# Optimization experiments

Measured on AMD Instinct MI355X. Metric: run time of the kernel, lower is better.

## Reference

```python
import jax, jax.numpy as jnp
import numpy as np
from jax import lax

COMMITMENT_COST = 0.25

def setup_inputs() -> dict:
    key = jax.random.key(0)
    k1, k2, k3, k4 = jax.random.split(key, 4)
    B, C, H, W, K = 32, 128, 32, 32, 8192
    return {
        "x": jax.random.normal(k1, (B, C, H, W), dtype=jnp.float32),
        "W_lin": jax.random.normal(k2, (C, C), dtype=jnp.float32) * (1.0 / np.sqrt(C)),
        "b_lin": jax.random.normal(k3, (C,), dtype=jnp.float32) * 0.01,
        "emb": jax.random.normal(k4, (K, C), dtype=jnp.float32),
    }

def reference(x, W_lin, b_lin, emb):
    B, C, H, W = x.shape
    K = emb.shape[0]
    # BCHW -> BHWC, then linear projection
    inp = jnp.transpose(x, (0, 2, 3, 1))          # [B,H,W,C]
    inp = inp @ W_lin.T + b_lin                   # nn.Linear
    flat = inp.reshape(-1, C)                     # [N,C], N=B*H*W
    # squared L2 distances to codebook: ||z||^2 + ||e||^2 - 2 z.e
    d = (jnp.sum(flat**2, axis=1, keepdims=True)
         + jnp.sum(emb**2, axis=1)
         - 2.0 * flat @ emb.T)                    # [N,K]
    idx = jnp.argmin(d, axis=1)                   # [N]
    quantized = emb[idx].reshape(inp.shape)       # gather == onehot @ emb
    e_latent = jnp.mean((lax.stop_gradient(quantized) - inp) ** 2)
    q_latent = jnp.mean((quantized - lax.stop_gradient(inp)) ** 2)
    loss = q_latent + COMMITMENT_COST * e_latent
    # straight-through estimator
    quantized_st = inp + lax.stop_gradient(quantized - inp)
    # perplexity from code usage histogram (== mean of one-hot encodings)
    counts = jnp.zeros((K,), dtype=flat.dtype).at[idx].add(1.0)
    avg_probs = counts / flat.shape[0]
    perplexity = jnp.exp(-jnp.sum(avg_probs * jnp.log(avg_probs + 1e-10)))
    out = jnp.transpose(quantized_st, (0, 3, 1, 2))  # back to BCHW
    return (loss, out, perplexity, idx[:, None])
```

## Files before the change

kernel.cpp:

```cpp
#include <hip/hip_runtime.h>
#include <hip/hip_bf16.h>
#include <float.h>

#define NPIX   32768
#define CDIM   128
#define KCB    8192
#define EPS_STOP 0.30f
#define TAUF   0.012f
#define RCAP   8192
#define RCAPA  2048

typedef _Float16 f16x8 __attribute__((ext_vector_type(8)));
typedef float    f32x16 __attribute__((ext_vector_type(16)));

#define WS_EMBFH   0
#define WS_E2      2359296
#define WS_ZWS     2392064
#define WS_CAND    19169280
#define WS_IDX     20217856
#define WS_RLISTA  20348928
#define WS_RLISTB  20381696
#define WS_SCAND   20512768
#define WS_SCANI   21037056
#define WS_COUNTS  21299200
#define WS_LOSS    21331968
#define WS_RCNTA   21331972
#define WS_RCNTB   21331976
#define WS_ZERO_OFF 21299200
#define WS_ZERO_LEN 32780

#define OUT_OFF_OUT  1
#define OUT_OFF_PERP 4194305
#define OUT_OFF_IDX  4194306

__device__ __forceinline__ void ins6(float f, float v[6]) {
    float a = fmaxf(v[0], f); v[0] = fminf(v[0], f);
    float b = fmaxf(v[1], a); v[1] = fminf(v[1], a);
    a = fmaxf(v[2], b); v[2] = fminf(v[2], b);
    b = fmaxf(v[3], a); v[3] = fminf(v[3], a);
    a = fmaxf(v[4], b); v[4] = fminf(v[4], b);
    v[5] = fminf(v[5], a);
}

__global__ __launch_bounds__(256) void k_e2(const float* __restrict__ emb, float* __restrict__ e2) {
    int t = threadIdx.x;
    int wv = t >> 6, l = t & 63;
    int k = blockIdx.x * 4 + wv;
    const float2 v = *(const float2*)&emb[(size_t)k * 128 + l * 2];
    float s = v.x * v.x + v.y * v.y;
    #pragma unroll
    for (int o = 32; o; o >>= 1) s += __shfl_down(s, o, 64);
    if (l == 0) e2[k] = s;
}

__global__ __launch_bounds__(256) void k_prep(const float* __restrict__ emb, const float* __restrict__ e2,
                                              _Float16* __restrict__ embFh) {
    int tid = blockIdx.x * 256 + threadIdx.x;
    int m = tid / 18, r = tid % 18;
    int s = r >> 1, h = r & 1;
    f16x8 hv;
    #pragma unroll
    for (int j = 0; j < 8; ++j) hv[j] = (_Float16)0.0f;
    if (s < 8) {
        int c0 = s * 16 + h * 8;
        const float4 a = *(const float4*)&emb[(size_t)m * 128 + c0];
        const float4 b = *(const float4*)&emb[(size_t)m * 128 + c0 + 4];
        float vals[8] = {a.x, a.y, a.z, a.w, b.x, b.y, b.z, b.w};
        #pragma unroll
        for (int j = 0; j < 8; ++j) hv[j] = (_Float16)(-2.0f * vals[j]);
    } else if (h == 0) {
        float v = e2[m] + 512.0f;
        _Float16 eh = (_Float16)v;
        hv[0] = eh;
        hv[1] = (_Float16)(v - (float)eh);
    }
    size_t base = (((size_t)(m >> 5) * 9 + s) * 64 + (m & 31) + h * 32) * 8;
    *(f16x8*)&embFh[base] = hv;
}

__global__ __launch_bounds__(256, 2) void k_main(
    const float* __restrict__ x, const float* __restrict__ Wl, const float* __restrict__ bl,
    const _Float16* __restrict__ embFh,
    float* __restrict__ zws, float4* __restrict__ cand)
{
    __shared__ __align__(16) float As[64 * 132];
    __shared__ __align__(16) float Xs[64 * 66];
    __shared__ float z2p[256];

    const int t  = threadIdx.x;
    const int n0 = blockIdx.x * 64;
    const int b  = n0 >> 10;
    const int hw0 = n0 & 1023;

    {
        const int p = t & 63, ig = t >> 6;
        float accz[32];
        const float4* bl4 = (const float4*)(bl + ig * 32);
        #pragma unroll
        for (int q = 0; q < 8; ++q) {
            float4 v = bl4[q];
            accz[4*q+0] = v.x; accz[4*q+1] = v.y; accz[4*q+2] = v.z; accz[4*q+3] = v.w;
        }
        for (int hf = 0; hf < 2; ++hf) {
            __syncthreads();
            for (int r = 0; r < 16; ++r) {
                int lin = r * 256 + t;
                int cc = lin >> 6, pp = lin & 63;
                Xs[cc * 66 + pp] = x[(size_t)(b * 128 + hf * 64 + cc) * 1024 + hw0 + pp];
            }
            __syncthreads();
            for (int cc4 = 0; cc4 < 16; ++cc4) {
                float xv0 = Xs[(cc4*4+0) * 66 + p];
                float xv1 = Xs[(cc4*4+1) * 66 + p];
                float xv2 = Xs[(cc4*4+2) * 66 + p];
                float xv3 = Xs[(cc4*4+3) * 66 + p];
                #pragma unroll
                for (int ii = 0; ii < 32; ++ii) {
                    const float4 w4 = *(const float4*)&Wl[(size_t)(ig*32+ii) * 128 + hf*64 + cc4*4];
                    float a = accz[ii];
                    a = fmaf(w4.x, xv0, a);
                    a = fmaf(w4.y, xv1, a);
                    a = fmaf(w4.z, xv2, a);
                    a = fmaf(w4.w, xv3, a);
                    accz[ii] = a;
                }
            }
        }
        float ssq = 0.f;
        float4* ao = (float4*)&As[p * 132 + ig * 32];
        float4* zo = (float4*)(zws + (size_t)(n0 + p) * 128 + ig * 32);
        #pragma unroll
        for (int q = 0; q < 8; ++q) {
            float4 v = make_float4(accz[4*q+0], accz[4*q+1], accz[4*q+2], accz[4*q+3]);
            ao[q] = v;
            zo[q] = v;
            ssq = fmaf(v.x, v.x, fmaf(v.y, v.y, fmaf(v.z, v.z, fmaf(v.w, v.w, ssq))));
        }
        z2p[p * 4 + ig] = ssq;
    }
    __syncthreads();

    const int l = t & 63, w = t >> 6;
    const int half = l >> 5, pcol = l & 31;
    f16x8 B0[9], B1[9];
    #pragma unroll
    for (int nt = 0; nt < 2; ++nt) {
        int p = nt * 32 + pcol;
        #pragma unroll
        for (int s = 0; s < 8; ++s) {
            const float* zp = &As[p * 132 + s * 16 + half * 8];
            float4 v0 = *(const float4*)zp;
            float4 v1 = *(const float4*)(zp + 4);
            float vals[8] = {v0.x, v0.y, v0.z, v0.w, v1.x, v1.y, v1.z, v1.w};
            f16x8 hh;
            #pragma unroll
            for (int j2 = 0; j2 < 8; ++j2) hh[j2] = (_Float16)vals[j2];
            if (nt == 0) B0[s] = hh; else B1[s] = hh;
        }
    }
    {
        f16x8 b8;
        #pragma unroll
        for (int j2 = 0; j2 < 8; ++j2) b8[j2] = (_Float16)0.0f;
        if (half == 0) { b8[0] = (_Float16)1.0f; b8[1] = (_Float16)1.0f; }
        B0[8] = b8; B1[8] = b8;
    }

    auto tree16 = [](const f32x16& v) -> float {
        float a = fminf(fminf(v[0], v[1]), fminf(v[2], v[3]));
        float bb = fminf(fminf(v[4], v[5]), fminf(v[6], v[7]));
        float c = fminf(fminf(v[8], v[9]), fminf(v[10], v[11]));
        float d = fminf(fminf(v[12], v[13]), fminf(v[14], v[15]));
        return fminf(fminf(a, bb), fminf(c, d));
    };

    float gv[6] = {3e38f, 3e38f, 3e38f, 3e38f, 3e38f, 3e38f};
    float hv[6] = {3e38f, 3e38f, 3e38f, 3e38f, 3e38f, 3e38f};
    const f16x8* Ahp = (const f16x8*)embFh;
    f16x8 aE[9], aO[9];
    {
        const f16x8* P = Ahp + (size_t)w * 576 + l;
        #pragma unroll
        for (int s = 0; s < 9; ++s) aE[s] = P[s * 64];
    }
    {
        const f16x8* P = Ahp + (size_t)(w + 4) * 576 + l;
        #pragma unroll
        for (int s = 0; s < 9; ++s) aO[s] = P[s * 64];
    }
    uint32_t idv = (uint32_t)((w << 1) | half);

    for (int g = w; g < 256; g += 8) {
        {
            f32x16 c00 = {}, c01 = {}, c10 = {}, c11 = {};
            #pragma unroll
            for (int s = 0; s < 9; ++s) {
                if (s & 1) {
                    c01 = __builtin_amdgcn_mfma_f32_32x32x16_f16(aE[s], B0[s], c01, 0, 0, 0);
                    c11 = __builtin_amdgcn_mfma_f32_32x32x16_f16(aE[s], B1[s], c11, 0, 0, 0);
                } else {
                    c00 = __builtin_amdgcn_mfma_f32_32x32x16_f16(aE[s], B0[s], c00, 0, 0, 0);
                    c10 = __builtin_amdgcn_mfma_f32_32x32x16_f16(aE[s], B1[s], c10, 0, 0, 0);
                }
            }
            f32x16 s0, s1;
            #pragma unroll
            for (int r = 0; r < 16; ++r) { s0[r] = c00[r] + c01[r]; s1[r] = c10[r] + c11[r]; }
            float m0 = tree16(s0), m1 = tree16(s1);
            ins6(__uint_as_float((__float_as_uint(m0) & 0xFFFFFE00u) | idv), gv);
            ins6(__uint_as_float((__float_as_uint(m1) & 0xFFFFFE00u) | idv), hv);
        }
        {
            int gn = (g + 8 < 256) ? (g + 8) : w;
            const f16x8* P = Ahp + (size_t)gn * 576 + l;
            #pragma unroll
            for (int s = 0; s < 9; ++s) aE[s] = P[s * 64];
        }
        {
            f32x16 c00 = {}, c01 = {}, c10 = {}, c11 = {};
            #pragma unroll
            for (int s = 0; s < 9; ++s) {
                if (s & 1) {
                    c01 = __builtin_amdgcn_mfma_f32_32x32x16_f16(aO[s], B0[s], c01, 0, 0, 0);
                    c11 = __builtin_amdgcn_mfma_f32_32x32x16_f16(aO[s], B1[s], c11, 0, 0, 0);
                } else {
                    c00 = __builtin_amdgcn_mfma_f32_32x32x16_f16(aO[s], B0[s], c00, 0, 0, 0);
                    c10 = __builtin_amdgcn_mfma_f32_32x32x16_f16(aO[s], B1[s], c10, 0, 0, 0);
                }
            }
            f32x16 s0, s1;
            #pragma unroll
            for (int r = 0; r < 16; ++r) { s0[r] = c00[r] + c01[r]; s1[r] = c10[r] + c11[r]; }
            float m0 = tree16(s0), m1 = tree16(s1);
            uint32_t ido = idv + 8u;
            ins6(__uint_as_float((__float_as_uint(m0) & 0xFFFFFE00u) | ido), gv);
            ins6(__uint_as_float((__float_as_uint(m1) & 0xFFFFFE00u) | ido), hv);
        }
        {
            int gn = (g + 12 < 256) ? (g + 12) : w;
            const f16x8* P = Ahp + (size_t)gn * 576 + l;
            #pragma unroll
            for (int s = 0; s < 9; ++s) aO[s] = P[s * 64];
        }
        idv += 16u;
    }

    __syncthreads();
    float* Ms = Xs;
    const int slot = (w << 1) | half;
    #pragma unroll
    for (int q = 0; q < 6; ++q) {
        Ms[(pcol * 8 + slot) * 6 + q] = gv[q];
        Ms[((32 + pcol) * 8 + slot) * 6 + q] = hv[q];
    }
    __syncthreads();
    if (t < 64) {
        float v6[6] = {3e38f, 3e38f, 3e38f, 3e38f, 3e38f, 3e38f};
        #pragma unroll
        for (int s = 0; s < 48; ++s) ins6(Ms[t * 48 + s], v6);
        float z2 = z2p[t*4+0] + z2p[t*4+1] + z2p[t*4+2] + z2p[t*4+3];
        cand[(size_t)(n0 + t) * 2 + 0] = make_float4(v6[0], v6[1], v6[2], v6[3]);
        cand[(size_t)(n0 + t) * 2 + 1] = make_float4(v6[4], v6[5], z2, 0.f);
    }
}

__global__ __launch_bounds__(256) void k_rec(
    const float* __restrict__ zws, const float* __restrict__ emb,
    const float4* __restrict__ cand, int* __restrict__ idxws,
    float* __restrict__ out_idxf, float* __restrict__ losssum,
    int* __restrict__ rlistA, int* __restrict__ rcntA,
    int* __restrict__ rlistB, int* __restrict__ rcntB)
{
    __shared__ float lred[16];
    const int t = threadIdx.x;
    const int pl = t >> 4, j = t & 15;
    const int n = blockIdx.x * 16 + pl;

    const float4 za = *(const float4*)&zws[(size_t)n * 128 + j * 8];
    const float4 zb = *(const float4*)&zws[(size_t)n * 128 + j * 8 + 4];
    const float4 c0 = cand[(size_t)n * 2 + 0];
    const float4 c1 = cand[(size_t)n * 2 + 1];
    const float pv[6] = {c0.x, c0.y, c0.z, c0.w, c1.x, c1.y};
    const float pbase = c1.z - 512.0f;

    float d1 = 3e38f, d2 = 3e38f; int i1 = 0x7fffffff, i2 = 0x7fffffff;
    bool safe = false;
    float lastgmin = 0.f;
    for (int q = 0; q < 6; ++q) {
        uint32_t bits = __float_as_uint(pv[q]);
        float gmin = __uint_as_float(bits & 0xFFFFFE00u);
        lastgmin = gmin;
        if (gmin >= d1 - pbase + EPS_STOP) { safe = true; break; }
        const int mbase = (int)((bits >> 1) & 255u) * 32 + (int)((bits & 1u) << 2);
        #pragma unroll
        for (int c = 0; c < 16; ++c) {
            int m = mbase + (c & 3) + 8 * (c >> 2);
            const float4 ea = *(const float4*)&emb[(size_t)m * 128 + j * 8];
            const float4 eb = *(const float4*)&emb[(size_t)m * 128 + j * 8 + 4];
            float da0 = za.x - ea.x, da1 = za.y - ea.y, da2 = za.z - ea.z, da3 = za.w - ea.w;
            float db0 = zb.x - eb.x, db1 = zb.y - eb.y, db2 = zb.z - eb.z, db3 = zb.w - eb.w;
            float s = da0*da0; s = fmaf(da1, da1, s); s = fmaf(da2, da2, s); s = fmaf(da3, da3, s);
            s = fmaf(db0, db0, s); s = fmaf(db1, db1, s); s = fmaf(db2, db2, s); s = fmaf(db3, db3, s);
            s += __shfl_xor(s, 1, 16);
            s += __shfl_xor(s, 2, 16);
            s += __shfl_xor(s, 4, 16);
            s += __shfl_xor(s, 8, 16);
            if (s < d1 || (s == d1 && m < i1)) { d2 = d1; i2 = i1; d1 = s; i1 = m; }
            else if (s < d2) { d2 = s; i2 = m; }
        }
    }
    if (!safe && lastgmin >= d1 - pbase + EPS_STOP) safe = true;

    if (j == 0) {
        idxws[n] = i1;
        out_idxf[n] = (float)i1;
        if (!safe) {
            int s = atomicAdd(rcntA, 1);
            if (s < RCAPA) rlistA[s] = n;
        } else if ((d2 - d1) < TAUF) {
            int s = atomicAdd(rcntB, 1);
            if (s < RCAP) { int4 v4 = make_int4(n, i1, i2, 0); ((int4*)rlistB)[s] = v4; }
        }
        lred[pl] = d1;
    }
    __syncthreads();
    if (t == 0) {
        float ls = 0.f;
        #pragma unroll
        for (int q = 0; q < 16; ++q) ls += lred[q];
        atomicAdd(losssum, ls);
    }
}

__global__ __launch_bounds__(256) void k_scanp(
    const float* __restrict__ zws, const float* __restrict__ emb,
    const int* __restrict__ rcntA, const int* __restrict__ rlistA,
    double* __restrict__ scand, int* __restrict__ scani)
{
    int cnt = *rcntA; if (cnt > RCAPA) cnt = RCAPA;
    const int t = threadIdx.x;
    const int chunk = blockIdx.x & 31;
    const int gi = t >> 4, j = t & 15;
    __shared__ double sd[16];
    __shared__ int si[16];
    for (int e = blockIdx.x >> 5; e < cnt; e += 64) {
        const int n = rlistA[e];
        const float4 za = *(const float4*)&zws[(size_t)n * 128 + j * 8];
        const float4 zb = *(const float4*)&zws[(size_t)n * 128 + j * 8 + 4];
        double best = 1e300; int bi = 0x7fffffff;
        const int kbase = chunk * 256 + gi * 16;
        for (int c = 0; c < 16; ++c) {
            const int m = kbase + c;
            const float4 ea = *(const float4*)&emb[(size_t)m * 128 + j * 8];
            const float4 eb = *(const float4*)&emb[(size_t)m * 128 + j * 8 + 4];
            double s = 0.0, d;
            d = (double)za.x - (double)ea.x; s += d * d;
            d = (double)za.y - (double)ea.y; s += d * d;
            d = (double)za.z - (double)ea.z; s += d * d;
            d = (double)za.w - (double)ea.w; s += d * d;
            d = (double)zb.x - (double)eb.x; s += d * d;
            d = (double)zb.y - (double)eb.y; s += d * d;
            d = (double)zb.z - (double)eb.z; s += d * d;
            d = (double)zb.w - (double)eb.w; s += d * d;
            s += __shfl_xor(s, 1, 16);
            s += __shfl_xor(s, 2, 16);
            s += __shfl_xor(s, 4, 16);
            s += __shfl_xor(s, 8, 16);
            if (s < best) { best = s; bi = m; }
        }
        __syncthreads();
        if (j == 0) { sd[gi] = best; si[gi] = bi; }
        __syncthreads();
        if (t == 0) {
            double b = sd[0]; int ib = si[0];
            #pragma unroll
            for (int q = 1; q < 16; ++q)
                if (sd[q] < b || (sd[q] == b && si[q] < ib)) { b = sd[q]; ib = si[q]; }
            scand[e * 32 + chunk] = b;
            scani[e * 32 + chunk] = ib;
        }
    }
}

__global__ __launch_bounds__(64) void k_mergeA(
    const int* __restrict__ rcntA, const int* __restrict__ rlistA,
    const double* __restrict__ scand, const int* __restrict__ scani,
    int* __restrict__ idxws, float* __restrict__ out_idxf)
{
    int cnt = *rcntA; if (cnt > RCAPA) cnt = RCAPA;
    const int t = threadIdx.x;
    for (int e = blockIdx.x; e < cnt; e += gridDim.x) {
        double b = 1e300; int ib = 0x7fffffff;
        if (t < 32) { b = scand[e * 32 + t]; ib = scani[e * 32 + t]; }
        #pragma unroll
        for (int o = 16; o; o >>= 1) {
            double ob = __shfl_down(b, o, 64);
            int oi = __shfl_down(ib, o, 64);
            if (ob < b || (ob == b && oi < ib)) { b = ob; ib = oi; }
        }
        if (t == 0) { int n = rlistA[e]; idxws[n] = ib; out_idxf[n] = (float)ib; }
    }
}

__global__ __launch_bounds__(128) void k_pairB(
    const float* __restrict__ x, const float* __restrict__ Wl, const float* __restrict__ bl,
    const float* __restrict__ emb, const int* __restrict__ rcntB, const int* __restrict__ rlistB,
    int* __restrict__ idxws, float* __restrict__ out_idxf)
{
    __shared__ double xs[128];
    __shared__ double red[128];
    int cnt = *rcntB; if (cnt > RCAP) cnt = RCAP;
    const int t = threadIdx.x;
    for (int e = blockIdx.x; e < cnt; e += gridDim.x) {
        const int4 v = ((const int4*)rlistB)[e];
        const int n = v.x, c1 = v.y, c2 = v.z;
        const int b = n >> 10, hw = n & 1023;
        __syncthreads();
        xs[t] = (double)x[(size_t)(b * 128 + t) * 1024 + hw];
        __syncthreads();
        double z = (double)bl[t];
        for (int c = 0; c < 128; ++c) z = fma((double)Wl[(size_t)t * 128 + c], xs[c], z);
        double d1v, d2v;
        double da = z - (double)emb[(size_t)c1 * 128 + t];
        red[t] = da * da; __syncthreads();
        for (int o = 64; o; o >>= 1) { if (t < o) red[t] += red[t + o]; __syncthreads(); }
        d1v = red[0]; __syncthreads();
        double db = z - (double)emb[(size_t)c2 * 128 + t];
        red[t] = db * db; __syncthreads();
        for (int o = 64; o; o >>= 1) { if (t < o) red[t] += red[t + o]; __syncthreads(); }
        d2v = red[0];
        if (t == 0) {
            int win = (d2v < d1v || (d2v == d1v && c2 < c1)) ? c2 : c1;
            idxws[n] = win;
            out_idxf[n] = (float)win;
        }
        __syncthreads();
    }
}

__global__ __launch_bounds__(256) void k_out(
    const float* __restrict__ emb, const int* __restrict__ idxws,
    float* __restrict__ outp , float* __restrict__ counts)
{
    const int t = threadIdx.x;
    const int b = blockIdx.x >> 2, h0 = (blockIdx.x & 3) << 3;
    const int n = b * 1024 + h0 * 32 + t;
    const int id = idxws[n];
    atomicAdd(&counts[id], 1.0f);
    const float4* ep = (const float4*)&emb[(size_t)id * 128];
    float* ob = outp + (size_t)b * 131072 + h0 * 32 + t;
    #pragma unroll 4
    for (int c4 = 0; c4 < 32; ++c4) {
        float4 v = ep[c4];
        ob[(c4 * 4 + 0) * 1024] = v.x;
        ob[(c4 * 4 + 1) * 1024] = v.y;
        ob[(c4 * 4 + 2) * 1024] = v.z;
        ob[(c4 * 4 + 3) * 1024] = v.w;
    }
}

__global__ __launch_bounds__(256) void k_final(
    const float* __restrict__ counts, const float* __restrict__ losssum, float* __restrict__ d_out)
{
    const int t = threadIdx.x;
    float ent = 0.f;
    for (int k = t; k < KCB; k += 256) {
        float p = counts[k] * (1.0f / 32768.0f);
        ent -= p * logf(p + 1e-10f);
    }
    #pragma unroll
    for (int o = 32; o; o >>= 1) ent += __shfl_down(ent, o, 64);
    __shared__ float wred[4];
    if ((t & 63) == 0) wred[t >> 6] = ent;
    __syncthreads();
    if (t == 0) {
        float e = wred[0] + wred[1] + wred[2] + wred[3];
        d_out[0] = 1.25f * (*losssum) * (1.0f / 4194304.0f);
        d_out[OUT_OFF_PERP] = expf(e);
    }
}

extern "C" void kernel_launch(void* const* d_in, const int* in_sizes, int n_in,
                              void* d_out, int out_size, void* d_ws, size_t ws_size,
                              hipStream_t stream) {
    (void)in_sizes; (void)n_in; (void)out_size; (void)ws_size;
    const float* x   = (const float*)d_in[0];
    const float* Wl  = (const float*)d_in[1];
    const float* bl  = (const float*)d_in[2];
    const float* emb = (const float*)d_in[3];
    float* out = (float*)d_out;
    char*  ws  = (char*)d_ws;

    _Float16* embFh = (_Float16*)(ws + WS_EMBFH);
    float* e2      = (float*)(ws + WS_E2);
    float* zws     = (float*)(ws + WS_ZWS);
    float4* cand   = (float4*)(ws + WS_CAND);
    int*   idxws   = (int*)  (ws + WS_IDX);
    int*   rlistA  = (int*)  (ws + WS_RLISTA);
    int*   rlistB  = (int*)  (ws + WS_RLISTB);
    double* scand  = (double*)(ws + WS_SCAND);
    int*   scani   = (int*)  (ws + WS_SCANI);
    float* counts  = (float*)(ws + WS_COUNTS);
    float* losssum = (float*)(ws + WS_LOSS);
    int*   rcntA   = (int*)  (ws + WS_RCNTA);
    int*   rcntB   = (int*)  (ws + WS_RCNTB);

    hipMemsetAsync(ws + WS_ZERO_OFF, 0, WS_ZERO_LEN, stream);

    k_e2<<<KCB / 4, 256, 0, stream>>>(emb, e2);
    k_prep<<<576, 256, 0, stream>>>(emb, e2, embFh);
    k_main<<<NPIX / 64, 256, 0, stream>>>(x, Wl, bl, embFh, zws, cand);
    k_rec<<<NPIX / 16, 256, 0, stream>>>(zws, emb, cand, idxws, out + OUT_OFF_IDX,
                                         losssum, rlistA, rcntA, rlistB, rcntB);
    k_scanp<<<2048, 256, 0, stream>>>(zws, emb, rcntA, rlistA, scand, scani);
    k_mergeA<<<32, 64, 0, stream>>>(rcntA, rlistA, scand, scani, idxws, out + OUT_OFF_IDX);
    k_pairB<<<256, 128, 0, stream>>>(x, Wl, bl, emb, rcntB, rlistB, idxws, out + OUT_OFF_IDX);
    k_out<<<128, 256, 0, stream>>>(emb, idxws, out + OUT_OFF_OUT, counts);
    k_final<<<1, 256, 0, stream>>>(counts, losssum, out);
}
```

Baseline: 312.1 us.

## Split k_main across 8 waves with one pixel tile per wave and higher occupancy

Moves k_main to 512-thread blocks. Each wave now computes distances for a single 32-pixel tile instead of two, which halves the per-wave B fragments and accumulators, and the launch bounds are raised to target more resident waves. The explicit double-buffered prefetch of codebook fragments is replaced by a plain load inside each iteration, and the MFMA sequence is wrapped with s_setprio. The tree min is restructured around a three-input min helper. In exchange, each codebook fragment is now fetched separately for each of the two pixel tiles, which doubles embedding reads, and the loss of explicit prefetch may expose load latency. The tight register budget implied by the launch bounds could also force spills.

```diff
diff --git a/kernel.cpp b/kernel.cpp
--- a/kernel.cpp
+++ b/kernel.cpp
@@ -33,6 +33,10 @@
 #define OUT_OFF_PERP 4194305
 #define OUT_OFF_IDX  4194306
 
+__device__ __forceinline__ float min3f(float a, float b, float c) {
+    return fminf(fminf(a, b), c);
+}
+
 __device__ __forceinline__ void ins6(float f, float v[6]) {
     float a = fmaxf(v[0], f); v[0] = fminf(v[0], f);
     float b = fmaxf(v[1], a); v[1] = fminf(v[1], a);
@@ -78,14 +82,14 @@
     *(f16x8*)&embFh[base] = hv;
 }
 
-__global__ __launch_bounds__(256, 2) void k_main(
+__global__ __launch_bounds__(512, 4) void k_main(
     const float* __restrict__ x, const float* __restrict__ Wl, const float* __restrict__ bl,
     const _Float16* __restrict__ embFh,
     float* __restrict__ zws, float4* __restrict__ cand)
 {
     __shared__ __align__(16) float As[64 * 132];
     __shared__ __align__(16) float Xs[64 * 66];
-    __shared__ float z2p[256];
+    __shared__ float z2p[64 * 8];
 
     const int t  = threadIdx.x;
     const int n0 = blockIdx.x * 64;
@@ -94,17 +98,17 @@
 
     {
         const int p = t & 63, ig = t >> 6;
-        float accz[32];
-        const float4* bl4 = (const float4*)(bl + ig * 32);
-        #pragma unroll
-        for (int q = 0; q < 8; ++q) {
+        float accz[16];
+        const float4* bl4 = (const float4*)(bl + ig * 16);
+        #pragma unroll
+        for (int q = 0; q < 4; ++q) {
             float4 v = bl4[q];
             accz[4*q+0] = v.x; accz[4*q+1] = v.y; accz[4*q+2] = v.z; accz[4*q+3] = v.w;
         }
         for (int hf = 0; hf < 2; ++hf) {
             __syncthreads();
-            for (int r = 0; r < 16; ++r) {
-                int lin = r * 256 + t;
+            for (int r = 0; r < 8; ++r) {
+                int lin = r * 512 + t;
                 int cc = lin >> 6, pp = lin & 63;
                 Xs[cc * 66 + pp] = x[(size_t)(b * 128 + hf * 64 + cc) * 1024 + hw0 + pp];
             }
@@ -115,8 +119,8 @@
                 float xv2 = Xs[(cc4*4+2) * 66 + p];
                 float xv3 = Xs[(cc4*4+3) * 66 + p];
                 #pragma unroll
-                for (int ii = 0; ii < 32; ++ii) {
-                    const float4 w4 = *(const float4*)&Wl[(size_t)(ig*32+ii) * 128 + hf*64 + cc4*4];
+                for (int ii = 0; ii < 16; ++ii) {
+                    const float4 w4 = *(const float4*)&Wl[(size_t)(ig*16+ii) * 128 + hf*64 + cc4*4];
                     float a = accz[ii];
                     a = fmaf(w4.x, xv0, a);
                     a = fmaf(w4.y, xv1, a);
@@ -127,138 +131,91 @@
             }
         }
         float ssq = 0.f;
-        float4* ao = (float4*)&As[p * 132 + ig * 32];
-        float4* zo = (float4*)(zws + (size_t)(n0 + p) * 128 + ig * 32);
-        #pragma unroll
-        for (int q = 0; q < 8; ++q) {
+        float4* ao = (float4*)&As[p * 132 + ig * 16];
+        float4* zo = (float4*)(zws + (size_t)(n0 + p) * 128 + ig * 16);
+        #pragma unroll
+        for (int q = 0; q < 4; ++q) {
             float4 v = make_float4(accz[4*q+0], accz[4*q+1], accz[4*q+2], accz[4*q+3]);
             ao[q] = v;
             zo[q] = v;
             ssq = fmaf(v.x, v.x, fmaf(v.y, v.y, fmaf(v.z, v.z, fmaf(v.w, v.w, ssq))));
         }
-        z2p[p * 4 + ig] = ssq;
+        z2p[p * 8 + ig] = ssq;
     }
     __syncthreads();
 
     const int l = t & 63, w = t >> 6;
     const int half = l >> 5, pcol = l & 31;
-    f16x8 B0[9], B1[9];
+    const int px = ((w >> 2) << 5) + pcol;
+    f16x8 B[9];
     #pragma unroll
-    for (int nt = 0; nt < 2; ++nt) {
-        int p = nt * 32 + pcol;
-        #pragma unroll
-        for (int s = 0; s < 8; ++s) {
-            const float* zp = &As[p * 132 + s * 16 + half * 8];
-            float4 v0 = *(const float4*)zp;
-            float4 v1 = *(const float4*)(zp + 4);
-            float vals[8] = {v0.x, v0.y, v0.z, v0.w, v1.x, v1.y, v1.z, v1.w};
-            f16x8 hh;
-            #pragma unroll
-            for (int j2 = 0; j2 < 8; ++j2) hh[j2] = (_Float16)vals[j2];
-            if (nt == 0) B0[s] = hh; else B1[s] = hh;
-        }
+    for (int s = 0; s < 8; ++s) {
+        const float* zp = &As[px * 132 + s * 16 + half * 8];
+        float4 v0 = *(const float4*)zp;
+        float4 v1 = *(const float4*)(zp + 4);
+        float vals[8] = {v0.x, v0.y, v0.z, v0.w, v1.x, v1.y, v1.z, v1.w};
+        f16x8 hh;
+        #pragma unroll
+        for (int j2 = 0; j2 < 8; ++j2) hh[j2] = (_Float16)vals[j2];
+        B[s] = hh;
     }
     {
         f16x8 b8;
         #pragma unroll
         for (int j2 = 0; j2 < 8; ++j2) b8[j2] = (_Float16)0.0f;
         if (half == 0) { b8[0] = (_Float16)1.0f; b8[1] = (_Float16)1.0f; }
-        B0[8] = b8; B1[8] = b8;
+        B[8] = b8;
     }
 
     auto tree16 = [](const f32x16& v) -> float {
-        float a = fminf(fminf(v[0], v[1]), fminf(v[2], v[3]));
-        float bb = fminf(fminf(v[4], v[5]), fminf(v[6], v[7]));
-        float c = fminf(fminf(v[8], v[9]), fminf(v[10], v[11]));
-        float d = fminf(fminf(v[12], v[13]), fminf(v[14], v[15]));
-        return fminf(fminf(a, bb), fminf(c, d));
+        float a = min3f(v[0], v[1], v[2]);
+        float bb = min3f(v[3], v[4], v[5]);
+        float c = min3f(v[6], v[7], v[8]);
+        float d = min3f(v[9], v[10], v[11]);
+        float e = min3f(v[12], v[13], v[14]);
+        float f = fminf(v[15], a);
+        return min3f(min3f(bb, c, d), e, f);
     };
 
     float gv[6] = {3e38f, 3e38f, 3e38f, 3e38f, 3e38f, 3e38f};
-    float hv[6] = {3e38f, 3e38f, 3e38f, 3e38f, 3e38f, 3e38f};
     const f16x8* Ahp = (const f16x8*)embFh;
-    f16x8 aE[9], aO[9];
-    {
-        const f16x8* P = Ahp + (size_t)w * 576 + l;
-        #pragma unroll
-        for (int s = 0; s < 9; ++s) aE[s] = P[s * 64];
-    }
-    {
-        const f16x8* P = Ahp + (size_t)(w + 4) * 576 + l;
-        #pragma unroll
-        for (int s = 0; s < 9; ++s) aO[s] = P[s * 64];
-    }
-    uint32_t idv = (uint32_t)((w << 1) | half);
-
-    for (int g = w; g < 256; g += 8) {
-        {
-            f32x16 c00 = {}, c01 = {}, c10 = {}, c11 = {};
-            #pragma unroll
-            for (int s = 0; s < 9; ++s) {
-                if (s & 1) {
-                    c01 = __builtin_amdgcn_mfma_f32_32x32x16_f16(aE[s], B0[s], c01, 0, 0, 0);
-                    c11 = __builtin_amdgcn_mfma_f32_32x32x16_f16(aE[s], B1[s], c11, 0, 0, 0);
-                } else {
-                    c00 = __builtin_amdgcn_mfma_f32_32x32x16_f16(aE[s], B0[s], c00, 0, 0, 0);
-                    c10 = __builtin_amdgcn_mfma_f32_32x32x16_f16(aE[s], B1[s], c10, 0, 0, 0);
-                }
-            }
-            f32x16 s0, s1;
-            #pragma unroll
-            for (int r = 0; r < 16; ++r) { s0[r] = c00[r] + c01[r]; s1[r] = c10[r] + c11[r]; }
-            float m0 = tree16(s0), m1 = tree16(s1);
-            ins6(__uint_as_float((__float_as_uint(m0) & 0xFFFFFE00u) | idv), gv);
-            ins6(__uint_as_float((__float_as_uint(m1) & 0xFFFFFE00u) | idv), hv);
-        }
-        {
-            int gn = (g + 8 < 256) ? (g + 8) : w;
-            const f16x8* P = Ahp + (size_t)gn * 576 + l;
-            #pragma unroll
-            for (int s = 0; s < 9; ++s) aE[s] = P[s * 64];
-        }
-        {
-            f32x16 c00 = {}, c01 = {}, c10 = {}, c11 = {};
-            #pragma unroll
-            for (int s = 0; s < 9; ++s) {
-                if (s & 1) {
-                    c01 = __builtin_amdgcn_mfma_f32_32x32x16_f16(aO[s], B0[s], c01, 0, 0, 0);
-                    c11 = __builtin_amdgcn_mfma_f32_32x32x16_f16(aO[s], B1[s], c11, 0, 0, 0);
-                } else {
-                    c00 = __builtin_amdgcn_mfma_f32_32x32x16_f16(aO[s], B0[s], c00, 0, 0, 0);
-                    c10 = __builtin_amdgcn_mfma_f32_32x32x16_f16(aO[s], B1[s], c10, 0, 0, 0);
-                }
-            }
-            f32x16 s0, s1;
-            #pragma unroll
-            for (int r = 0; r < 16; ++r) { s0[r] = c00[r] + c01[r]; s1[r] = c10[r] + c11[r]; }
-            float m0 = tree16(s0), m1 = tree16(s1);
-            uint32_t ido = idv + 8u;
-            ins6(__uint_as_float((__float_as_uint(m0) & 0xFFFFFE00u) | ido), gv);
-            ins6(__uint_as_float((__float_as_uint(m1) & 0xFFFFFE00u) | ido), hv);
-        }
-        {
-            int gn = (g + 12 < 256) ? (g + 12) : w;
-            const f16x8* P = Ahp + (size_t)gn * 576 + l;
-            #pragma unroll
-            for (int s = 0; s < 9; ++s) aO[s] = P[s * 64];
-        }
-        idv += 16u;
+
+    for (int g = (w & 3); g < 256; g += 4) {
+        const f16x8* P = Ahp + (size_t)g * 576 + l;
+        f16x8 a[9];
+        #pragma unroll
+        for (int s = 0; s < 9; ++s) a[s] = P[s * 64];
+
+        f32x16 c00 = {}, c01 = {};
+        __builtin_amdgcn_s_setprio(1);
+        #pragma unroll
+        for (int s = 0; s < 9; ++s) {
+            if (s & 1) c01 = __builtin_amdgcn_mfma_f32_32x32x16_f16(a[s], B[s], c01, 0, 0, 0);
+            else       c00 = __builtin_amdgcn_mfma_f32_32x32x16_f16(a[s], B[s], c00, 0, 0, 0);
+        }
+        __builtin_amdgcn_s_setprio(0);
+
+        f32x16 s0;
+        #pragma unroll
+        for (int r = 0; r < 16; ++r) s0[r] = c00[r] + c01[r];
+        float m0 = tree16(s0);
+        uint32_t id = (uint32_t)((g << 1) | half);
+        ins6(__uint_as_float((__float_as_uint(m0) & 0xFFFFFE00u) | id), gv);
     }
 
     __syncthreads();
     float* Ms = Xs;
-    const int slot = (w << 1) | half;
+    const int slot = ((w & 3) << 1) | half;
     #pragma unroll
-    for (int q = 0; q < 6; ++q) {
-        Ms[(pcol * 8 + slot) * 6 + q] = gv[q];
-        Ms[((32 + pcol) * 8 + slot) * 6 + q] = hv[q];
-    }
+    for (int q = 0; q < 6; ++q) Ms[(px * 8 + slot) * 6 + q] = gv[q];
     __syncthreads();
     if (t < 64) {
         float v6[6] = {3e38f, 3e38f, 3e38f, 3e38f, 3e38f, 3e38f};
         #pragma unroll
         for (int s = 0; s < 48; ++s) ins6(Ms[t * 48 + s], v6);
-        float z2 = z2p[t*4+0] + z2p[t*4+1] + z2p[t*4+2] + z2p[t*4+3];
+        float z2 = 0.f;
+        #pragma unroll
+        for (int q = 0; q < 8; ++q) z2 += z2p[t * 8 + q];
         cand[(size_t)(n0 + t) * 2 + 0] = make_float4(v6[0], v6[1], v6[2], v6[3]);
         cand[(size_t)(n0 + t) * 2 + 1] = make_float4(v6[4], v6[5], z2, 0.f);
     }
@@ -509,7 +466,7 @@
 
     k_e2<<<KCB / 4, 256, 0, stream>>>(emb, e2);
     k_prep<<<576, 256, 0, stream>>>(emb, e2, embFh);
-    k_main<<<NPIX / 64, 256, 0, stream>>>(x, Wl, bl, embFh, zws, cand);
+    k_main<<<NPIX / 64, 512, 0, stream>>>(x, Wl, bl, embFh, zws, cand);
     k_rec<<<NPIX / 16, 256, 0, stream>>>(zws, emb, cand, idxws, out + OUT_OFF_IDX,
                                          losssum, rlistA, rcntA, rlistB, rcntB);
     k_scanp<<<2048, 256, 0, stream>>>(zws, emb, rcntA, rlistA, scand, scani);
```

Result: no change. 318.1 us (+1.9%).
